# Performance work log

Measured on AMD Instinct MI355X. Metric: run time of the kernel, lower is better.

The kernel has to match this reference:

```python
import jax, jax.numpy as jnp
import numpy as np

NEG = -1e10


def trilinear_attn(C, Q, w4C, w4Q, w4mlu, bias):
    # C: [B,Lc,d], Q: [B,Lq,d]
    sub0 = C @ w4C                      # [B,Lc,1]
    sub1 = jnp.swapaxes(Q @ w4Q, 1, 2)  # [B,1,Lq]
    sub2 = jnp.einsum('bcd,bqd->bcq', C * w4mlu, Q)  # [B,Lc,Lq]
    return sub0 + sub1 + sub2 + bias


def setup_inputs() -> dict:
    key = jax.random.key(0)
    k1, k2, k3, k4, k5 = jax.random.split(key, 5)
    B, Lc, Lq, d = 16, 2048, 512, 128
    C = jax.random.normal(k1, (B, Lc, d), dtype=jnp.float32)
    Q = jax.random.normal(k2, (B, Lq, d), dtype=jnp.float32)
    Cmask = jnp.ones((B, Lc), dtype=bool)
    Qmask = jnp.ones((B, Lq), dtype=bool)
    # xavier_uniform for [d,1]: bound = sqrt(6/(d+1))
    bC = float(np.sqrt(6.0 / (d + 1)))
    w4C = jax.random.uniform(k3, (d, 1), minval=-bC, maxval=bC, dtype=jnp.float32)
    w4Q = jax.random.uniform(k4, (d, 1), minval=-bC, maxval=bC, dtype=jnp.float32)
    # xavier for [1,1,d]: fan_in=1*d? torch treats dims>2: fan_in = size(1)*size(2)=d, fan_out = size(0)*size(2)=d
    bM = float(np.sqrt(6.0 / (d + d)))
    w4mlu = jax.random.uniform(k5, (1, 1, d), minval=-bM, maxval=bM, dtype=jnp.float32)
    bias = jnp.zeros((1,), dtype=jnp.float32)
    return {"C": C, "Q": Q, "Cmask": Cmask, "Qmask": Qmask,
            "w4C": w4C, "w4Q": w4Q, "w4mlu": w4mlu, "bias": bias}


def reference(C, Q, Cmask, Qmask, w4C, w4Q, w4mlu, bias):
    B, Lc, _ = C.shape
    Lq = Q.shape[1]
    cm = Cmask.astype(jnp.float32).reshape(B, Lc, 1)
    qm = Qmask.astype(jnp.float32).reshape(B, 1, Lq)
    S = trilinear_attn(C, Q, w4C, w4Q, w4mlu, bias)  # [B,Lc,Lq]
    S1 = jax.nn.softmax(S * qm + (1.0 - qm) * NEG, axis=2)
    S2 = jax.nn.softmax(S * cm + (1.0 - cm) * NEG, axis=1)
    A = jnp.einsum('bcq,bqd->bcd', S1, Q)                    # [B,Lc,d]
    S12 = jnp.einsum('bcq,bkq->bck', S1, S2)                 # S1 @ S2^T, [B,Lc,Lc]
    Bt = jnp.einsum('bck,bkd->bcd', S12, C)                  # [B,Lc,d]
    return jnp.concatenate([C, A, C * A, C * Bt], axis=2)
```

## Files before the change

kernel.cpp:

```cpp
#include <hip/hip_runtime.h>

#define B_  16
#define LC  2048
#define LQ  512
#define DD  128
#define L2E 1.44269504088896340736f
#define SP  16

typedef __attribute__((ext_vector_type(8))) short bf16x8;
typedef __attribute__((ext_vector_type(4))) float f32x4;
typedef unsigned short u16;
typedef unsigned int   u32;

#define MFMA(a,b,c) __builtin_amdgcn_mfma_f32_16x16x32_bf16((a),(b),(c),0,0,0)

__device__ __forceinline__ u16 f2bf(float x){
  u32 u = __builtin_bit_cast(u32, x);
  u32 r = (u + 0x7FFFu + ((u >> 16) & 1u)) >> 16;
  return (u16)r;
}
__device__ __forceinline__ float bf2f(u16 h){
  u32 u = ((u32)h) << 16;
  return __builtin_bit_cast(float, u);
}
__device__ __forceinline__ bf16x8 ldb8(const u16* p){
  return *reinterpret_cast<const bf16x8*>(p);
}
__device__ __forceinline__ const u16* swz(const u16* base, int row, int colb){
  return base + (row << 7) + ((colb ^ ((row & 7) << 4)) >> 1);
}
#define GLOAD_LDS(g, l) \
  __builtin_amdgcn_global_load_lds((const __attribute__((address_space(1))) void*)(g), \
                                   (__attribute__((address_space(3))) void*)(l), 16, 0, 0)

__global__ void prep(const float* __restrict__ C, const float* __restrict__ Q,
                     const float* __restrict__ w4C, const float* __restrict__ w4Q,
                     const float* __restrict__ w4mlu,
                     u16* __restrict__ Cb,  u16* __restrict__ CbT,
                     u16* __restrict__ Qwb, u16* __restrict__ QbT,
                     float* __restrict__ sub0, float* __restrict__ sub1){
  __shared__ u16 tile[64][130];
  __shared__ float wl[128];
  int t = threadIdx.x, blk = blockIdx.x;
  int lane = t & 63;
  bool isC = blk < 512;
  if (t < 128) wl[t] = w4mlu[t];
  __syncthreads();
  float2 wv = reinterpret_cast<const float2*>(isC ? w4C : w4Q)[lane];
  if (isC) {
    int b = blk >> 5, ct = blk & 31, c0 = ct << 6;
    const float* src = C + ((size_t)(b*LC + c0))*DD;
    for (int k = 0; k < 16; ++k) {
      int idx = t + (k << 8);
      int r = idx >> 6, d2 = idx & 63;
      float2 v = reinterpret_cast<const float2*>(src + (size_t)r*DD)[d2];
      float sdot = v.x*wv.x + v.y*wv.y;
      #pragma unroll
      for (int o = 32; o > 0; o >>= 1) sdot += __shfl_xor(sdot, o);
      if (lane == 0) sub0[b*LC + c0 + r] = sdot;
      u16 h0 = f2bf(v.x), h1 = f2bf(v.y);
      size_t o = ((size_t)(b*LC + c0 + r))*DD + 2*d2;
      *reinterpret_cast<u32*>(Cb + o) = (u32)h0 | ((u32)h1 << 16);
      tile[r][2*d2]   = h0;
      tile[r][2*d2+1] = h1;
    }
    __syncthreads();
    for (int k = 0; k < 8; ++k) {
      int ch = t + (k << 8);
      int d = ch >> 4, c4 = (ch & 15) << 2;
      u32 lo = (u32)tile[c4][d]   | ((u32)tile[c4+1][d] << 16);
      u32 hi = (u32)tile[c4+2][d] | ((u32)tile[c4+3][d] << 16);
      uint2 u; u.x = lo; u.y = hi;
      *reinterpret_cast<uint2*>(CbT + ((size_t)(b*DD + d))*LC + c0 + c4) = u;
    }
  } else {
    int bq = blk - 512;
    int b = bq >> 3, qt = bq & 7, q0 = qt << 6;
    const float* src = Q + ((size_t)(b*LQ + q0))*DD;
    for (int k = 0; k < 16; ++k) {
      int idx = t + (k << 8);
      int r = idx >> 6, d2 = idx & 63;
      float2 v = reinterpret_cast<const float2*>(src + (size_t)r*DD)[d2];
      float sdot = v.x*wv.x + v.y*wv.y;
      #pragma unroll
      for (int o = 32; o > 0; o >>= 1) sdot += __shfl_xor(sdot, o);
      if (lane == 0) sub1[b*LQ + q0 + r] = sdot;
      float qw0 = v.x * wl[2*d2], qw1 = v.y * wl[2*d2+1];
      size_t o = ((size_t)(b*LQ + q0 + r))*DD + 2*d2;
      *reinterpret_cast<u32*>(Qwb + o) = (u32)f2bf(qw0) | ((u32)f2bf(qw1) << 16);
      tile[r][2*d2]   = f2bf(v.x);
      tile[r][2*d2+1] = f2bf(v.y);
    }
    __syncthreads();
    for (int k = 0; k < 8; ++k) {
      int ch = t + (k << 8);
      int d = ch >> 4, c4 = (ch & 15) << 2;
      u32 lo = (u32)tile[c4][d]   | ((u32)tile[c4+1][d] << 16);
      u32 hi = (u32)tile[c4+2][d] | ((u32)tile[c4+3][d] << 16);
      uint2 u; u.x = lo; u.y = hi;
      *reinterpret_cast<uint2*>(QbT + ((size_t)(b*DD + d))*LQ + q0 + c4) = u;
    }
  }
}

__global__ __launch_bounds__(256, 3)
void flashT(const u16* __restrict__ Qwb, const u16* __restrict__ Cb,
            const u16* __restrict__ CbT, const float* __restrict__ sub0,
            float* __restrict__ mPart, float* __restrict__ lPart,
            u16* __restrict__ TaccP){
  __shared__ __align__(16) u16 buf[128*128];
  __shared__ u16 Pl[64][136];
  int bid = blockIdx.x;
  int id = (bid & 7) * 256 + (bid >> 3);
  int b = id >> 7, qb = (id >> 4) & 7, sp = id & 15;
  int c0 = sp * 128;
  int w = threadIdx.x >> 6, l = threadIdx.x & 63;
  int lj = l & 15, lg = l >> 4;

  {
    const char* gb = (const char*)(Cb + ((size_t)(b*LC + c0))*DD);
    #pragma unroll
    for (int i = 0; i < 8; ++i) {
      int off = (w*8 + i)*1024 + l*16;
      int row = off >> 8, col = off & 255;
      int src = (row << 8) | (col ^ ((row & 7) << 4));
      GLOAD_LDS(gb + src, (char*)buf + off);
    }
  }
  const u16* Qrow = Qwb + ((size_t)(b*LQ + qb*64 + w*16 + lj))*DD;
  bf16x8 aq[4];
  #pragma unroll
  for (int k = 0; k < 4; ++k) aq[k] = ldb8(Qrow + k*32 + lg*8);
  float s0v[8];
  #pragma unroll
  for (int f = 0; f < 8; ++f) s0v[f] = sub0[b*LC + c0 + f*16 + lj];
  __syncthreads();

  f32x4 s[8];
  #pragma unroll
  for (int f = 0; f < 8; ++f) s[f] = (f32x4){0.f,0.f,0.f,0.f};
  #pragma unroll
  for (int ks = 0; ks < 4; ++ks) {
    #pragma unroll
    for (int f = 0; f < 8; ++f)
      s[f] = MFMA(aq[ks], ldb8(swz(buf, f*16 + lj, ks*64 + lg*16)), s[f]);
  }
  __syncthreads();

  {
    const char* gb = (const char*)CbT + ((size_t)b*DD)*LC*2 + (size_t)c0*2;
    #pragma unroll
    for (int i = 0; i < 8; ++i) {
      int off = (w*8 + i)*1024 + l*16;
      int row = off >> 8, col = off & 255;
      size_t src = (size_t)row*(LC*2) + (col ^ ((row & 7) << 4));
      GLOAD_LDS(gb + src, (char*)buf + off);
    }
  }

  float tm[4] = {-1e30f,-1e30f,-1e30f,-1e30f};
  #pragma unroll
  for (int f = 0; f < 8; ++f) {
    #pragma unroll
    for (int r = 0; r < 4; ++r) { s[f][r] += s0v[f]; tm[r] = fmaxf(tm[r], s[f][r]); }
  }
  #pragma unroll
  for (int r = 0; r < 4; ++r) {
    #pragma unroll
    for (int m = 1; m < 16; m <<= 1) tm[r] = fmaxf(tm[r], __shfl_xor(tm[r], m));
  }
  float psum[4] = {0.f,0.f,0.f,0.f};
  #pragma unroll
  for (int f = 0; f < 8; ++f) {
    #pragma unroll
    for (int r = 0; r < 4; ++r) {
      float p = exp2f((s[f][r] - tm[r]) * L2E);
      psum[r] += p;
      Pl[w*16 + lg*4 + r][f*16 + lj] = f2bf(p);
    }
  }
  #pragma unroll
  for (int r = 0; r < 4; ++r) {
    #pragma unroll
    for (int m = 1; m < 16; m <<= 1) psum[r] += __shfl_xor(psum[r], m);
  }
  int pbase = (b*8 + qb)*SP + sp;
  if (lj == 0) {
    #pragma unroll
    for (int r = 0; r < 4; ++r) {
      mPart[pbase*64 + w*16 + lg*4 + r] = tm[r];
      lPart[pbase*64 + w*16 + lg*4 + r] = psum[r];
    }
  }
  __syncthreads();

  f32x4 tacc[8];
  #pragma unroll
  for (int f = 0; f < 8; ++f) tacc[f] = (f32x4){0.f,0.f,0.f,0.f};
  #pragma unroll
  for (int ks = 0; ks < 4; ++ks) {
    bf16x8 ap = *reinterpret_cast<const bf16x8*>(&Pl[w*16 + lj][ks*32 + lg*8]);
    #pragma unroll
    for (int f = 0; f < 8; ++f)
      tacc[f] = MFMA(ap, ldb8(swz(buf, f*16 + lj, ks*64 + lg*16)), tacc[f]);
  }
  #pragma unroll
  for (int f = 0; f < 8; ++f) {
    ushort4 hv;
    hv.x = f2bf(tacc[f][0]); hv.y = f2bf(tacc[f][1]);
    hv.z = f2bf(tacc[f][2]); hv.w = f2bf(tacc[f][3]);
    *reinterpret_cast<ushort4*>(TaccP + (((size_t)pbase*4 + w)*8 + f)*256 + lj*16 + lg*4) = hv;
  }
}

__global__ void combineT(const float* __restrict__ mPart, const float* __restrict__ lPart,
                         const u16* __restrict__ TaccP, u16* __restrict__ TbT){
  __shared__ float fac[SP][64];
  __shared__ u16 Tt[64][68];
  int blk = blockIdx.x;
  int b = blk >> 4, qb = (blk >> 1) & 7, dh = blk & 1;
  int t = threadIdx.x;
  int base = (b*8 + qb)*SP;
  if (t < 64) {
    float m_[SP], mm = -1e30f;
    #pragma unroll
    for (int p = 0; p < SP; ++p) { m_[p] = mPart[(base+p)*64 + t]; mm = fmaxf(mm, m_[p]); }
    float lt = 0.f, e[SP];
    #pragma unroll
    for (int p = 0; p < SP; ++p) {
      e[p] = exp2f((m_[p] - mm) * L2E);
      lt += lPart[(base+p)*64 + t] * e[p];
    }
    float il = 1.0f / lt;
    #pragma unroll
    for (int p = 0; p < SP; ++p) fac[p][t] = e[p] * il;
  }
  __syncthreads();
  int lj = t >> 4, lg = (t >> 2) & 3, r = t & 3;
  for (int w = 0; w < 4; ++w) {
    int q = w*16 + lg*4 + r;
    for (int fi = 0; fi < 4; ++fi) {
      int f = dh*4 + fi;
      float acc = 0.f;
      #pragma unroll
      for (int p = 0; p < SP; ++p)
        acc += bf2f(TaccP[(((size_t)(base+p)*4 + w)*8 + f)*256 + t]) * fac[p][q];
      Tt[q][fi*16 + lj] = f2bf(acc);
    }
  }
  __syncthreads();
  for (int k = 0; k < 4; ++k) {
    int ch = t + (k << 8); int dl = ch >> 4, q4 = (ch & 15) << 2;
    u32 lo = (u32)Tt[q4][dl]   | ((u32)Tt[q4+1][dl] << 16);
    u32 hi = (u32)Tt[q4+2][dl] | ((u32)Tt[q4+3][dl] << 16);
    uint2 u; u.x = lo; u.y = hi;
    *reinterpret_cast<uint2*>(TbT + ((size_t)(b*DD + dh*64 + dl))*LQ + qb*64 + q4) = u;
  }
}

__global__ __launch_bounds__(256, 2)
void rowflash(const float* __restrict__ Cf, const u16* __restrict__ Cb,
              const u16* __restrict__ Qwb, const u16* __restrict__ QbT,
              const u16* __restrict__ TbT, const float* __restrict__ sub1,
              float* __restrict__ out){
  __shared__ __align__(16) char smem[57344];
  char* sQw = smem;
  char* sQt = smem + 16384;
  char* sTt = smem + 32768;
  char* sPl = smem + 49152;

  int bid = blockIdx.x;
  int id = (bid & 7) * 64 + (bid >> 3);
  int b = id >> 5, ct = id & 31, c0 = ct * 64;
  int tid = threadIdx.x;
  int w = tid >> 6, l = tid & 63;
  int lj = l & 15, lg = l >> 4;

  const char* gQw = (const char*)Qwb + (size_t)(b*LQ)*256;
  const char* gQt = (const char*)QbT + (size_t)(b*DD)*1024;
  const char* gTt = (const char*)TbT + (size_t)(b*DD)*1024;

  bf16x8 ca[4];
  #pragma unroll
  for (int ks = 0; ks < 4; ++ks)
    ca[ks] = ldb8(Cb + ((size_t)(b*LC + c0 + w*16 + lj))*DD + ks*32 + lg*8);

  #pragma unroll
  for (int i = 0; i < 4; ++i) {
    int off = i*4096 + tid*16;
    { int row = off >> 8, col = off & 255;
      GLOAD_LDS(gQw + (size_t)row*256 + (col ^ ((row & 7) << 4)), sQw + off); }
    { int row = off >> 7, col = off & 127;
      size_t src = (size_t)row*1024 + (col ^ ((row & 7) << 4));
      GLOAD_LDS(gQt + src, sQt + off);
      GLOAD_LDS(gTt + src, sTt + off); }
  }

  float mrun = -1e30f, lrun = 0.f;
  f32x4 aA[8], aB[8];
  #pragma unroll
  for (int df = 0; df < 8; ++df) { aA[df] = (f32x4){0.f,0.f,0.f,0.f}; aB[df] = (f32x4){0.f,0.f,0.f,0.f}; }

  int crow = w*16 + lj;
  __syncthreads();

  for (int ch = 0; ch < 8; ++ch) {
    f32x4 s4[4];
    #pragma unroll
    for (int qf = 0; qf < 4; ++qf) s4[qf] = (f32x4){0.f,0.f,0.f,0.f};
    #pragma unroll
    for (int qf = 0; qf < 4; ++qf) {
      int qr = qf*16 + lj;
      #pragma unroll
      for (int ks = 0; ks < 4; ++ks) {
        bf16x8 aq = ldb8((const u16*)(sQw + qr*256 + ((ks*64 + lg*16) ^ ((qr & 7) << 4))));
        s4[qf] = MFMA(aq, ca[ks], s4[qf]);
      }
    }
    float tm = -1e30f;
    #pragma unroll
    for (int qf = 0; qf < 4; ++qf) {
      f32x4 sv = *reinterpret_cast<const f32x4*>(sub1 + b*LQ + ch*64 + qf*16 + lg*4);
      s4[qf] += sv;
      #pragma unroll
      for (int r = 0; r < 4; ++r) tm = fmaxf(tm, s4[qf][r]);
    }
    tm = fmaxf(tm, __shfl_xor(tm, 16));
    tm = fmaxf(tm, __shfl_xor(tm, 32));
    float mn = fmaxf(mrun, tm);
    float fsc = exp2f((mrun - mn) * L2E);
    mrun = mn;
    lrun *= fsc;
    #pragma unroll
    for (int df = 0; df < 8; ++df) { aA[df] *= fsc; aB[df] *= fsc; }
    float psum = 0.f;
    #pragma unroll
    for (int qf = 0; qf < 4; ++qf) {
      ushort4 hv;
      #pragma unroll
      for (int r = 0; r < 4; ++r) {
        float p = exp2f((s4[qf][r] - mrun) * L2E);
        psum += p;
        ((u16*)&hv)[r] = f2bf(p);
      }
      *reinterpret_cast<ushort4*>(sPl + crow*128 + ((qf*32 + lg*8) ^ ((crow & 7) << 4))) = hv;
    }
    psum += __shfl_xor(psum, 16);
    psum += __shfl_xor(psum, 32);
    lrun += psum;

    __syncthreads();
    if (ch < 7) {
      #pragma unroll
      for (int i = 0; i < 4; ++i) {
        int off = i*4096 + tid*16, row = off >> 8, col = off & 255;
        GLOAD_LDS(gQw + (size_t)(ch+1)*16384 + row*256 + (col ^ ((row & 7) << 4)), sQw + off);
      }
    }
    bf16x8 pb[2];
    #pragma unroll
    for (int ks2 = 0; ks2 < 2; ++ks2)
      pb[ks2] = ldb8((const u16*)(sPl + crow*128 + ((ks2*64 + lg*16) ^ ((crow & 7) << 4))));
    #pragma unroll
    for (int df = 0; df < 8; ++df) {
      int dr = df*16 + lj;
      int sw = (dr & 7) << 4;
      #pragma unroll
      for (int ks2 = 0; ks2 < 2; ++ks2) {
        int cb = (ks2*64 + lg*16) ^ sw;
        bf16x8 at = ldb8((const u16*)(sQt + dr*128 + cb));
        aA[df] = MFMA(at, pb[ks2], aA[df]);
        bf16x8 bt = ldb8((const u16*)(sTt + dr*128 + cb));
        aB[df] = MFMA(bt, pb[ks2], aB[df]);
      }
    }
    __syncthreads();
    if (ch < 7) {
      #pragma unroll
      for (int i = 0; i < 4; ++i) {
        int off = i*4096 + tid*16, row = off >> 7, col = off & 127;
        size_t src = (size_t)row*1024 + (ch+1)*128 + (col ^ ((row & 7) << 4));
        GLOAD_LDS(gQt + src, sQt + off);
        GLOAD_LDS(gTt + src, sTt + off);
      }
    }
  }

  float linv = 1.0f / lrun;
  size_t rowb = (size_t)(b*LC + c0 + w*16 + lj);
  const float4* cfp = reinterpret_cast<const float4*>(Cf + rowb*DD);
  float4* op = reinterpret_cast<float4*>(out + rowb*512);
  #pragma unroll
  for (int df = 0; df < 8; ++df) {
    int dq = df*4 + lg;
    float4 Cv = cfp[dq];
    float4 Av, Bv, CA, CB;
    Av.x = aA[df][0]*linv; Av.y = aA[df][1]*linv; Av.z = aA[df][2]*linv; Av.w = aA[df][3]*linv;
    Bv.x = aB[df][0]*linv; Bv.y = aB[df][1]*linv; Bv.z = aB[df][2]*linv; Bv.w = aB[df][3]*linv;
    CA.x = Cv.x*Av.x; CA.y = Cv.y*Av.y; CA.z = Cv.z*Av.z; CA.w = Cv.w*Av.w;
    CB.x = Cv.x*Bv.x; CB.y = Cv.y*Bv.y; CB.z = Cv.z*Bv.z; CB.w = Cv.w*Bv.w;
    op[dq]      = Cv;
    op[32 + dq] = Av;
    op[64 + dq] = CA;
    op[96 + dq] = CB;
  }
}

extern "C" void kernel_launch(void* const* d_in, const int* in_sizes, int n_in,
                              void* d_out, int out_size, void* d_ws, size_t ws_size,
                              hipStream_t stream) {
  const float* C     = (const float*)d_in[0];
  const float* Q     = (const float*)d_in[1];
  const float* w4C   = (const float*)d_in[4];
  const float* w4Q   = (const float*)d_in[5];
  const float* w4mlu = (const float*)d_in[6];
  float* out = (float*)d_out;

  char* ws = (char*)d_ws;
  size_t off = 0;
  auto alloc = [&](size_t bytes) -> void* {
    void* p = ws + off;
    off += (bytes + 255) & ~(size_t)255;
    return p;
  };
  float* sub0  = (float*)alloc((size_t)B_*LC*4);
  float* sub1  = (float*)alloc((size_t)B_*LQ*4);
  u16*   Cb    = (u16*)  alloc((size_t)B_*LC*DD*2);
  u16*   CbT   = (u16*)  alloc((size_t)B_*DD*LC*2);
  u16*   Qwb   = (u16*)  alloc((size_t)B_*LQ*DD*2);
  u16*   QbT   = (u16*)  alloc((size_t)B_*DD*LQ*2);
  u16*   TbT   = (u16*)  alloc((size_t)B_*DD*LQ*2);
  float* mPart = (float*)alloc((size_t)B_*8*SP*64*4);
  float* lPart = (float*)alloc((size_t)B_*8*SP*64*4);
  u16*   TaccP = (u16*)  alloc((size_t)B_*8*SP*64*DD*2);

  hipLaunchKernelGGL(prep, dim3(640), dim3(256), 0, stream,
                     C, Q, w4C, w4Q, w4mlu, Cb, CbT, Qwb, QbT, sub0, sub1);
  hipLaunchKernelGGL(flashT, dim3(2048), dim3(256), 0, stream,
                     Qwb, Cb, CbT, sub0, mPart, lPart, TaccP);
  hipLaunchKernelGGL(combineT, dim3(256), dim3(256), 0, stream,
                     mPart, lPart, TaccP, TbT);
  hipLaunchKernelGGL(rowflash, dim3(512), dim3(256), 0, stream,
                     C, Cb, Qwb, QbT, TbT, sub1, out);
}
```

Before: 85.98 us.

## Reuse C tiles across four Q chunks in flashT and add lazy rescale

flashT now loads both the C and C-transposed tiles into LDS once per block and loops over four 64-row Q chunks, so the grid drops from 2048 to 512 blocks and each C tile is reused instead of reloaded for every Q chunk. The LDS swizzle changes to a 16-row XOR pattern in flashT and rowflash, and the transposed Q/T tiles in rowflash are repacked to 256-byte rows. MFMA sections are wrapped in s_setprio. rowflash skips the online-softmax rescale unless the running max grows by more than 8, which saves the multiplies on the accumulators. The cost is 80 KB of LDS per flashT block, occupancy lowered to 2 blocks per unit, fewer blocks to spread across the device, and a small risk of reduced numerical headroom from the lazy rescale.

```diff
diff --git a/kernel.cpp b/kernel.cpp
--- a/kernel.cpp
+++ b/kernel.cpp
@@ -25,9 +25,6 @@
 }
 __device__ __forceinline__ bf16x8 ldb8(const u16* p){
   return *reinterpret_cast<const bf16x8*>(p);
-}
-__device__ __forceinline__ const u16* swz(const u16* base, int row, int colb){
-  return base + (row << 7) + ((colb ^ ((row & 7) << 4)) >> 1);
 }
 #define GLOAD_LDS(g, l) \
   __builtin_amdgcn_global_load_lds((const __attribute__((address_space(1))) void*)(g), \
@@ -103,113 +100,123 @@
   }
 }
 
-__global__ __launch_bounds__(256, 3)
+__global__ __launch_bounds__(256, 2)
 void flashT(const u16* __restrict__ Qwb, const u16* __restrict__ Cb,
             const u16* __restrict__ CbT, const float* __restrict__ sub0,
             float* __restrict__ mPart, float* __restrict__ lPart,
             u16* __restrict__ TaccP){
-  __shared__ __align__(16) u16 buf[128*128];
-  __shared__ u16 Pl[64][136];
+  __shared__ __align__(16) char smem[81920];
+  char* bufC  = smem;
+  char* bufCT = smem + 32768;
+  char* Plb   = smem + 65536;
   int bid = blockIdx.x;
-  int id = (bid & 7) * 256 + (bid >> 3);
-  int b = id >> 7, qb = (id >> 4) & 7, sp = id & 15;
+  int id = (bid & 7) * 64 + (bid >> 3);
+  int b = id >> 5, qh = (id >> 4) & 1, sp = id & 15;
   int c0 = sp * 128;
-  int w = threadIdx.x >> 6, l = threadIdx.x & 63;
+  int tid = threadIdx.x;
+  int w = tid >> 6, l = tid & 63;
   int lj = l & 15, lg = l >> 4;
 
   {
-    const char* gb = (const char*)(Cb + ((size_t)(b*LC + c0))*DD);
+    const char* gc = (const char*)(Cb + ((size_t)(b*LC + c0))*DD);
+    const char* gt = (const char*)CbT + ((size_t)(b*DD))*LC*2 + (size_t)c0*2;
     #pragma unroll
     for (int i = 0; i < 8; ++i) {
-      int off = (w*8 + i)*1024 + l*16;
+      int off = i*4096 + tid*16;
       int row = off >> 8, col = off & 255;
-      int src = (row << 8) | (col ^ ((row & 7) << 4));
-      GLOAD_LDS(gb + src, (char*)buf + off);
-    }
-  }
-  const u16* Qrow = Qwb + ((size_t)(b*LQ + qb*64 + w*16 + lj))*DD;
-  bf16x8 aq[4];
-  #pragma unroll
-  for (int k = 0; k < 4; ++k) aq[k] = ldb8(Qrow + k*32 + lg*8);
+      int sc = col ^ ((row & 15) << 4);
+      GLOAD_LDS(gc + (size_t)row*256 + sc, bufC + off);
+      GLOAD_LDS(gt + (size_t)row*(LC*2) + sc, bufCT + off);
+    }
+  }
   float s0v[8];
   #pragma unroll
   for (int f = 0; f < 8; ++f) s0v[f] = sub0[b*LC + c0 + f*16 + lj];
   __syncthreads();
 
-  f32x4 s[8];
-  #pragma unroll
-  for (int f = 0; f < 8; ++f) s[f] = (f32x4){0.f,0.f,0.f,0.f};
-  #pragma unroll
-  for (int ks = 0; ks < 4; ++ks) {
-    #pragma unroll
-    for (int f = 0; f < 8; ++f)
-      s[f] = MFMA(aq[ks], ldb8(swz(buf, f*16 + lj, ks*64 + lg*16)), s[f]);
-  }
-  __syncthreads();
-
-  {
-    const char* gb = (const char*)CbT + ((size_t)b*DD)*LC*2 + (size_t)c0*2;
-    #pragma unroll
-    for (int i = 0; i < 8; ++i) {
-      int off = (w*8 + i)*1024 + l*16;
-      int row = off >> 8, col = off & 255;
-      size_t src = (size_t)row*(LC*2) + (col ^ ((row & 7) << 4));
-      GLOAD_LDS(gb + src, (char*)buf + off);
-    }
-  }
-
-  float tm[4] = {-1e30f,-1e30f,-1e30f,-1e30f};
-  #pragma unroll
-  for (int f = 0; f < 8; ++f) {
-    #pragma unroll
-    for (int r = 0; r < 4; ++r) { s[f][r] += s0v[f]; tm[r] = fmaxf(tm[r], s[f][r]); }
-  }
-  #pragma unroll
-  for (int r = 0; r < 4; ++r) {
-    #pragma unroll
-    for (int m = 1; m < 16; m <<= 1) tm[r] = fmaxf(tm[r], __shfl_xor(tm[r], m));
-  }
-  float psum[4] = {0.f,0.f,0.f,0.f};
-  #pragma unroll
-  for (int f = 0; f < 8; ++f) {
+  for (int qch = 0; qch < 4; ++qch) {
+    int q0 = qh*256 + qch*64;
+    const u16* Qrow = Qwb + ((size_t)(b*LQ + q0 + w*16 + lj))*DD;
+    bf16x8 aq[4];
+    #pragma unroll
+    for (int ks = 0; ks < 4; ++ks) aq[ks] = ldb8(Qrow + ks*32 + lg*8);
+
+    f32x4 s[8];
+    #pragma unroll
+    for (int f = 0; f < 8; ++f) s[f] = (f32x4){0.f,0.f,0.f,0.f};
+    __builtin_amdgcn_s_setprio(1);
+    #pragma unroll
+    for (int ks = 0; ks < 4; ++ks) {
+      #pragma unroll
+      for (int f = 0; f < 8; ++f) {
+        int row = f*16 + lj;
+        s[f] = MFMA(aq[ks],
+                    ldb8((const u16*)(bufC + row*256 + ((ks*64 + lg*16) ^ (lj << 4)))),
+                    s[f]);
+      }
+    }
+    __builtin_amdgcn_s_setprio(0);
+
+    float tm[4] = {-1e30f,-1e30f,-1e30f,-1e30f};
+    #pragma unroll
+    for (int f = 0; f < 8; ++f) {
+      #pragma unroll
+      for (int r = 0; r < 4; ++r) { s[f][r] += s0v[f]; tm[r] = fmaxf(tm[r], s[f][r]); }
+    }
     #pragma unroll
     for (int r = 0; r < 4; ++r) {
-      float p = exp2f((s[f][r] - tm[r]) * L2E);
-      psum[r] += p;
-      Pl[w*16 + lg*4 + r][f*16 + lj] = f2bf(p);
-    }
-  }
-  #pragma unroll
-  for (int r = 0; r < 4; ++r) {
-    #pragma unroll
-    for (int m = 1; m < 16; m <<= 1) psum[r] += __shfl_xor(psum[r], m);
-  }
-  int pbase = (b*8 + qb)*SP + sp;
-  if (lj == 0) {
+      #pragma unroll
+      for (int m = 1; m < 16; m <<= 1) tm[r] = fmaxf(tm[r], __shfl_xor(tm[r], m));
+    }
+    float psum[4] = {0.f,0.f,0.f,0.f};
+    #pragma unroll
+    for (int f = 0; f < 8; ++f) {
+      #pragma unroll
+      for (int r = 0; r < 4; ++r) {
+        float p = exp2f((s[f][r] - tm[r]) * L2E);
+        psum[r] += p;
+        int qp = w*16 + lg*4 + r;
+        *(u16*)(Plb + qp*256 + ((f*32 + lj*2) ^ ((qp & 15) << 4))) = f2bf(p);
+      }
+    }
     #pragma unroll
     for (int r = 0; r < 4; ++r) {
-      mPart[pbase*64 + w*16 + lg*4 + r] = tm[r];
-      lPart[pbase*64 + w*16 + lg*4 + r] = psum[r];
-    }
-  }
-  __syncthreads();
-
-  f32x4 tacc[8];
-  #pragma unroll
-  for (int f = 0; f < 8; ++f) tacc[f] = (f32x4){0.f,0.f,0.f,0.f};
-  #pragma unroll
-  for (int ks = 0; ks < 4; ++ks) {
-    bf16x8 ap = *reinterpret_cast<const bf16x8*>(&Pl[w*16 + lj][ks*32 + lg*8]);
-    #pragma unroll
-    for (int f = 0; f < 8; ++f)
-      tacc[f] = MFMA(ap, ldb8(swz(buf, f*16 + lj, ks*64 + lg*16)), tacc[f]);
-  }
-  #pragma unroll
-  for (int f = 0; f < 8; ++f) {
-    ushort4 hv;
-    hv.x = f2bf(tacc[f][0]); hv.y = f2bf(tacc[f][1]);
-    hv.z = f2bf(tacc[f][2]); hv.w = f2bf(tacc[f][3]);
-    *reinterpret_cast<ushort4*>(TaccP + (((size_t)pbase*4 + w)*8 + f)*256 + lj*16 + lg*4) = hv;
+      #pragma unroll
+      for (int m = 1; m < 16; m <<= 1) psum[r] += __shfl_xor(psum[r], m);
+    }
+    int pbase = (b*8 + qh*4 + qch)*SP + sp;
+    if (lj == 0) {
+      #pragma unroll
+      for (int r = 0; r < 4; ++r) {
+        mPart[pbase*64 + w*16 + lg*4 + r] = tm[r];
+        lPart[pbase*64 + w*16 + lg*4 + r] = psum[r];
+      }
+    }
+
+    f32x4 tacc[8];
+    #pragma unroll
+    for (int f = 0; f < 8; ++f) tacc[f] = (f32x4){0.f,0.f,0.f,0.f};
+    __builtin_amdgcn_s_setprio(1);
+    #pragma unroll
+    for (int ks = 0; ks < 4; ++ks) {
+      int prow = w*16 + lj;
+      bf16x8 ap = ldb8((const u16*)(Plb + prow*256 + ((ks*64 + lg*16) ^ ((prow & 15) << 4))));
+      #pragma unroll
+      for (int f = 0; f < 8; ++f) {
+        int drow = f*16 + lj;
+        tacc[f] = MFMA(ap,
+                       ldb8((const u16*)(bufCT + drow*256 + ((ks*64 + lg*16) ^ (lj << 4)))),
+                       tacc[f]);
+      }
+    }
+    __builtin_amdgcn_s_setprio(0);
+    #pragma unroll
+    for (int f = 0; f < 8; ++f) {
+      ushort4 hv;
+      hv.x = f2bf(tacc[f][0]); hv.y = f2bf(tacc[f][1]);
+      hv.z = f2bf(tacc[f][2]); hv.w = f2bf(tacc[f][3]);
+      *reinterpret_cast<ushort4*>(TaccP + (((size_t)pbase*4 + w)*8 + f)*256 + lj*16 + lg*4) = hv;
+    }
   }
 }
 
@@ -289,9 +296,12 @@
   for (int i = 0; i < 4; ++i) {
     int off = i*4096 + tid*16;
     { int row = off >> 8, col = off & 255;
-      GLOAD_LDS(gQw + (size_t)row*256 + (col ^ ((row & 7) << 4)), sQw + off); }
-    { int row = off >> 7, col = off & 127;
-      size_t src = (size_t)row*1024 + (col ^ ((row & 7) << 4));
+      GLOAD_LDS(gQw + (size_t)row*256 + (col ^ ((row & 15) << 4)), sQw + off); }
+    { int R = off >> 8, colp = off & 255;
+      int colb = colp ^ ((R & 15) << 4);
+      int d = R + ((colb >> 7) << 6);
+      int qoff = colb & 127;
+      size_t src = (size_t)d*1024 + qoff;
       GLOAD_LDS(gQt + src, sQt + off);
       GLOAD_LDS(gTt + src, sTt + off); }
   }
@@ -308,15 +318,18 @@
     f32x4 s4[4];
     #pragma unroll
     for (int qf = 0; qf < 4; ++qf) s4[qf] = (f32x4){0.f,0.f,0.f,0.f};
+    __builtin_amdgcn_s_setprio(1);
     #pragma unroll
     for (int qf = 0; qf < 4; ++qf) {
       int qr = qf*16 + lj;
       #pragma unroll
       for (int ks = 0; ks < 4; ++ks) {
-        bf16x8 aq = ldb8((const u16*)(sQw + qr*256 + ((ks*64 + lg*16) ^ ((qr & 7) << 4))));
+        bf16x8 aq = ldb8((const u16*)(sQw + qr*256 + ((ks*64 + lg*16) ^ (lj << 4))));
         s4[qf] = MFMA(aq, ca[ks], s4[qf]);
       }
     }
+    __builtin_amdgcn_s_setprio(0);
+
     float tm = -1e30f;
     #pragma unroll
     for (int qf = 0; qf < 4; ++qf) {
@@ -327,12 +340,14 @@
     }
     tm = fmaxf(tm, __shfl_xor(tm, 16));
     tm = fmaxf(tm, __shfl_xor(tm, 32));
-    float mn = fmaxf(mrun, tm);
-    float fsc = exp2f((mrun - mn) * L2E);
-    mrun = mn;
-    lrun *= fsc;
-    #pragma unroll
-    for (int df = 0; df < 8; ++df) { aA[df] *= fsc; aB[df] *= fsc; }
+    if (!__all(tm - mrun <= 8.0f)) {
+      float mn = fmaxf(mrun, tm);
+      float fsc = exp2f((mrun - mn) * L2E);
+      lrun *= fsc;
+      #pragma unroll
+      for (int df = 0; df < 8; ++df) { aA[df] *= fsc; aB[df] *= fsc; }
+      mrun = mn;
+    }
     float psum = 0.f;
     #pragma unroll
     for (int qf = 0; qf < 4; ++qf) {
@@ -354,32 +369,39 @@
       #pragma unroll
       for (int i = 0; i < 4; ++i) {
         int off = i*4096 + tid*16, row = off >> 8, col = off & 255;
-        GLOAD_LDS(gQw + (size_t)(ch+1)*16384 + row*256 + (col ^ ((row & 7) << 4)), sQw + off);
+        GLOAD_LDS(gQw + (size_t)(ch+1)*16384 + row*256 + (col ^ ((row & 15) << 4)), sQw + off);
       }
     }
     bf16x8 pb[2];
     #pragma unroll
     for (int ks2 = 0; ks2 < 2; ++ks2)
       pb[ks2] = ldb8((const u16*)(sPl + crow*128 + ((ks2*64 + lg*16) ^ ((crow & 7) << 4))));
+    __builtin_amdgcn_s_setprio(1);
     #pragma unroll
     for (int df = 0; df < 8; ++df) {
       int dr = df*16 + lj;
-      int sw = (dr & 7) << 4;
+      int R = dr & 63;
+      int hb = (dr >> 6) << 7;
       #pragma unroll
       for (int ks2 = 0; ks2 < 2; ++ks2) {
-        int cb = (ks2*64 + lg*16) ^ sw;
-        bf16x8 at = ldb8((const u16*)(sQt + dr*128 + cb));
+        int byte = R*256 + ((hb + ks2*64 + lg*16) ^ ((R & 15) << 4));
+        bf16x8 at = ldb8((const u16*)(sQt + byte));
         aA[df] = MFMA(at, pb[ks2], aA[df]);
-        bf16x8 bt = ldb8((const u16*)(sTt + dr*128 + cb));
+        bf16x8 bt = ldb8((const u16*)(sTt + byte));
         aB[df] = MFMA(bt, pb[ks2], aB[df]);
       }
     }
+    __builtin_amdgcn_s_setprio(0);
     __syncthreads();
     if (ch < 7) {
       #pragma unroll
       for (int i = 0; i < 4; ++i) {
-        int off = i*4096 + tid*16, row = off >> 7, col = off & 127;
-        size_t src = (size_t)row*1024 + (ch+1)*128 + (col ^ ((row & 7) << 4));
+        int off = i*4096 + tid*16;
+        int R = off >> 8, colp = off & 255;
+        int colb = colp ^ ((R & 15) << 4);
+        int d = R + ((colb >> 7) << 6);
+        int qoff = colb & 127;
+        size_t src = (size_t)d*1024 + (size_t)(ch+1)*128 + qoff;
         GLOAD_LDS(gQt + src, sQt + off);
         GLOAD_LDS(gTt + src, sTt + off);
       }
@@ -436,7 +458,7 @@
 
   hipLaunchKernelGGL(prep, dim3(640), dim3(256), 0, stream,
                      C, Q, w4C, w4Q, w4mlu, Cb, CbT, Qwb, QbT, sub0, sub1);
-  hipLaunchKernelGGL(flashT, dim3(2048), dim3(256), 0, stream,
+  hipLaunchKernelGGL(flashT, dim3(512), dim3(256), 0, stream,
                      Qwb, Cb, CbT, sub0, mPart, lPart, TaccP);
   hipLaunchKernelGGL(combineT, dim3(256), dim3(256), 0, stream,
                      mPart, lPart, TaccP, TbT);
```

New measurement: 120.3 us. +39.9%, slower.

## Rework LDS swizzle layout, add MFMA priority hints and lazy softmax rescale

Applied to the files above, without the earlier changes.

Changes the LDS layout of the Qw and transposed Q/T tiles to a 256-byte-row, 16-way XOR swizzle, packing two 64-row halves per row, which is meant to reduce bank conflicts on the MFMA operand loads. Wraps the two MFMA loops in s_setprio hints so waves issuing matrix work are scheduled ahead of others. Skips the online-softmax rescale of the accumulators unless some lane's chunk max exceeds the running max by more than 8. That lazy rescale avoids many vector multiplies but lets exponentials grow up to e^8 before renormalisation, which relies on fp32 and bf16 range headroom.

```diff
diff --git a/kernel.cpp b/kernel.cpp
--- a/kernel.cpp
+++ b/kernel.cpp
@@ -289,9 +289,12 @@
   for (int i = 0; i < 4; ++i) {
     int off = i*4096 + tid*16;
     { int row = off >> 8, col = off & 255;
-      GLOAD_LDS(gQw + (size_t)row*256 + (col ^ ((row & 7) << 4)), sQw + off); }
-    { int row = off >> 7, col = off & 127;
-      size_t src = (size_t)row*1024 + (col ^ ((row & 7) << 4));
+      GLOAD_LDS(gQw + (size_t)row*256 + (col ^ ((row & 15) << 4)), sQw + off); }
+    { int R = off >> 8, colp = off & 255;
+      int colb = colp ^ ((R & 15) << 4);
+      int d = R + ((colb >> 7) << 6);
+      int qoff = colb & 127;
+      size_t src = (size_t)d*1024 + qoff;
       GLOAD_LDS(gQt + src, sQt + off);
       GLOAD_LDS(gTt + src, sTt + off); }
   }
@@ -308,15 +311,18 @@
     f32x4 s4[4];
     #pragma unroll
     for (int qf = 0; qf < 4; ++qf) s4[qf] = (f32x4){0.f,0.f,0.f,0.f};
+    __builtin_amdgcn_s_setprio(1);
     #pragma unroll
     for (int qf = 0; qf < 4; ++qf) {
       int qr = qf*16 + lj;
       #pragma unroll
       for (int ks = 0; ks < 4; ++ks) {
-        bf16x8 aq = ldb8((const u16*)(sQw + qr*256 + ((ks*64 + lg*16) ^ ((qr & 7) << 4))));
+        bf16x8 aq = ldb8((const u16*)(sQw + qr*256 + ((ks*64 + lg*16) ^ (lj << 4))));
         s4[qf] = MFMA(aq, ca[ks], s4[qf]);
       }
     }
+    __builtin_amdgcn_s_setprio(0);
+
     float tm = -1e30f;
     #pragma unroll
     for (int qf = 0; qf < 4; ++qf) {
@@ -327,12 +333,14 @@
     }
     tm = fmaxf(tm, __shfl_xor(tm, 16));
     tm = fmaxf(tm, __shfl_xor(tm, 32));
-    float mn = fmaxf(mrun, tm);
-    float fsc = exp2f((mrun - mn) * L2E);
-    mrun = mn;
-    lrun *= fsc;
-    #pragma unroll
-    for (int df = 0; df < 8; ++df) { aA[df] *= fsc; aB[df] *= fsc; }
+    if (!__all(tm - mrun <= 8.0f)) {
+      float mn = fmaxf(mrun, tm);
+      float fsc = exp2f((mrun - mn) * L2E);
+      lrun *= fsc;
+      #pragma unroll
+      for (int df = 0; df < 8; ++df) { aA[df] *= fsc; aB[df] *= fsc; }
+      mrun = mn;
+    }
     float psum = 0.f;
     #pragma unroll
     for (int qf = 0; qf < 4; ++qf) {
@@ -354,32 +362,39 @@
       #pragma unroll
       for (int i = 0; i < 4; ++i) {
         int off = i*4096 + tid*16, row = off >> 8, col = off & 255;
-        GLOAD_LDS(gQw + (size_t)(ch+1)*16384 + row*256 + (col ^ ((row & 7) << 4)), sQw + off);
+        GLOAD_LDS(gQw + (size_t)(ch+1)*16384 + row*256 + (col ^ ((row & 15) << 4)), sQw + off);
       }
     }
     bf16x8 pb[2];
     #pragma unroll
     for (int ks2 = 0; ks2 < 2; ++ks2)
       pb[ks2] = ldb8((const u16*)(sPl + crow*128 + ((ks2*64 + lg*16) ^ ((crow & 7) << 4))));
+    __builtin_amdgcn_s_setprio(1);
     #pragma unroll
     for (int df = 0; df < 8; ++df) {
       int dr = df*16 + lj;
-      int sw = (dr & 7) << 4;
+      int R = dr & 63;
+      int hb = (dr >> 6) << 7;
       #pragma unroll
       for (int ks2 = 0; ks2 < 2; ++ks2) {
-        int cb = (ks2*64 + lg*16) ^ sw;
-        bf16x8 at = ldb8((const u16*)(sQt + dr*128 + cb));
+        int byte = R*256 + ((hb + ks2*64 + lg*16) ^ ((R & 15) << 4));
+        bf16x8 at = ldb8((const u16*)(sQt + byte));
         aA[df] = MFMA(at, pb[ks2], aA[df]);
-        bf16x8 bt = ldb8((const u16*)(sTt + dr*128 + cb));
+        bf16x8 bt = ldb8((const u16*)(sTt + byte));
         aB[df] = MFMA(bt, pb[ks2], aB[df]);
       }
     }
+    __builtin_amdgcn_s_setprio(0);
     __syncthreads();
     if (ch < 7) {
       #pragma unroll
       for (int i = 0; i < 4; ++i) {
-        int off = i*4096 + tid*16, row = off >> 7, col = off & 127;
-        size_t src = (size_t)row*1024 + (ch+1)*128 + (col ^ ((row & 7) << 4));
+        int off = i*4096 + tid*16;
+        int R = off >> 8, colp = off & 255;
+        int colb = colp ^ ((R & 15) << 4);
+        int d = R + ((colb >> 7) << 6);
+        int qoff = colb & 127;
+        size_t src = (size_t)d*1024 + (size_t)(ch+1)*128 + qoff;
         GLOAD_LDS(gQt + src, sQt + off);
         GLOAD_LDS(gTt + src, sTt + off);
       }
```

Measured after the change: 86.22 us. Within noise of the previous version (+0.3%).
